# Performance work log

Measured on AMD Instinct MI355X. Metric: run time of the kernel, lower is better.

## Reference

```python
import jax, jax.numpy as jnp
import numpy as np

N_NODES = 50000


def _gcn_norm(edge_index, num_nodes):
    # PyG GCNConv default: add self-loops, symmetric deg^{-1/2} normalization.
    src, dst = edge_index[0], edge_index[1]
    loops = jnp.arange(num_nodes, dtype=src.dtype)
    src = jnp.concatenate([src, loops])
    dst = jnp.concatenate([dst, loops])
    ones = jnp.ones(src.shape[0], dtype=jnp.float32)
    deg = jax.ops.segment_sum(ones, dst, num_segments=num_nodes)
    dinv = jnp.where(deg > 0, jax.lax.rsqrt(deg), 0.0)
    norm = dinv[src] * dinv[dst]  # [E + N]
    return src, dst, norm


def _gcn_layer(x, src, dst, norm, W, b, num_nodes):
    h = x @ W                                   # [N, H]
    msg = h[src] * norm[:, None]                # gather + scale, [E+N, H]
    out = jax.ops.segment_sum(msg, dst, num_segments=num_nodes)  # scatter-add
    return out + b


def setup_inputs() -> dict:
    key = jax.random.key(0)
    ks = jax.random.split(key, 8)
    d_in, d_h = 128, 128
    x = jax.random.normal(ks[0], (N_NODES, d_in), dtype=jnp.float32)
    edge_index = jax.random.randint(ks[1], (2, 800000), 0, N_NODES, dtype=jnp.int64)
    s1 = 1.0 / np.sqrt(d_in)
    s2 = 1.0 / np.sqrt(d_h)
    W1 = jax.random.normal(ks[2], (d_in, d_h), dtype=jnp.float32) * s1
    b1 = jnp.zeros((d_h,), dtype=jnp.float32)
    W2 = jax.random.normal(ks[3], (d_h, d_h), dtype=jnp.float32) * s2
    b2 = jnp.zeros((d_h,), dtype=jnp.float32)
    Wl = jax.random.normal(ks[4], (d_h, 1), dtype=jnp.float32) * s2
    bl = jnp.zeros((1,), dtype=jnp.float32)
    return {"x": x, "edge_index": edge_index, "W1": W1, "b1": b1,
            "W2": W2, "b2": b2, "Wl": Wl, "bl": bl}


def reference(x, edge_index, W1, b1, W2, b2, Wl, bl):
    n = x.shape[0]
    src, dst, norm = _gcn_norm(edge_index, n)
    h = jax.nn.relu(_gcn_layer(x, src, dst, norm, W1, b1, n))
    # dropout is identity in eval mode
    h = _gcn_layer(h, src, dst, norm, W2, b2, n)
    return jax.nn.sigmoid(h @ Wl + bl)  # [N, 1]
```

## Files before the change

kernel.cpp:

```cpp
#include <hip/hip_runtime.h>
#include <math.h>

#define NN 50000
#define NE 800000
#define DD 128
#define NPAD 50048
#define NSLICE 6256
#define ELLW 64

typedef __attribute__((ext_vector_type(8))) short bf16x8;
typedef __attribute__((ext_vector_type(4))) float f32x4;

__device__ __forceinline__ int clampN(int v) {
  return v < 0 ? 0 : (v >= NN ? NN - 1 : v);
}

__device__ __forceinline__ unsigned short f2b(float f) {
  union { float f; unsigned int u; } x; x.f = f;
  unsigned int u = x.u;
  u += 0x7fffu + ((u >> 16) & 1u);
  return (unsigned short)(u >> 16);
}

__device__ __forceinline__ float blo(unsigned int v) {
  union { unsigned int u; float f; } a; a.u = v << 16; return a.f;
}
__device__ __forceinline__ float bhi(unsigned int v) {
  union { unsigned int u; float f; } a; a.u = v & 0xffff0000u; return a.f;
}


__global__ __launch_bounds__(256) void k_scatter_ell(
    const int* __restrict__ ei, int* __restrict__ cur, int* __restrict__ col) {
  int g = blockIdx.x & 7;
  int blk = blockIdx.x >> 3;
  int lo = g * NSLICE;
  int hi = min(lo + NSLICE, NN);
  for (int i = blk * 256 + threadIdx.x; i < NE; i += 256 * 256) {
    int d = clampN(ei[NE + i]);
    if (d >= lo && d < hi) {
      int s = clampN(ei[i]);
      int pos = atomicAdd(&cur[d], 1);
      if (pos < ELLW) col[d * ELLW + pos] = s;
    }
  }
}

__global__ void k_dinv(const int* __restrict__ cur, float* __restrict__ dinv, int n) {
  int i = blockIdx.x * blockDim.x + threadIdx.x;
  if (i < n) dinv[i] = rsqrtf(1.0f + (float)cur[i]);
}


__global__ __launch_bounds__(256) void k_prep_w(
    const float* __restrict__ W1, const float* __restrict__ W2,
    const float* __restrict__ b2, const float* __restrict__ Wl,
    const float* __restrict__ bl, unsigned short* __restrict__ Wt1,
    float* __restrict__ w2l, float* __restrict__ c0b) {
  __shared__ float part[2];
  if (blockIdx.x < 64) {
    int i = blockIdx.x * 256 + threadIdx.x;
    int n = i >> 7, k = i & 127;
    Wt1[i] = f2b(W1[k * DD + n]);
  } else if (threadIdx.x < DD) {
    int k = threadIdx.x;
    float acc = 0.f;
    for (int c = 0; c < DD; ++c) acc += W2[k * DD + c] * Wl[c];
    w2l[k] = acc;
    float pc = b2[k] * Wl[k];
#pragma unroll
    for (int off = 32; off > 0; off >>= 1) pc += __shfl_down(pc, off, 64);
    if ((k & 63) == 0) part[k >> 6] = pc;
    __syncthreads();
    if (k == 0) c0b[0] = part[0] + part[1] + bl[0];
  }
}


__global__ __launch_bounds__(256) void k_gemm_f32(
    const float* __restrict__ x, const unsigned short* __restrict__ Wt,
    const float* __restrict__ dinv, unsigned short* __restrict__ outb) {
  __shared__ char lds[16384 + 32768];
  char* Al = lds;
  char* Wl = lds + 16384;

  const int tid = threadIdx.x;
  const int row0 = blockIdx.x * 64;

  {
    const float4* src = (const float4*)x;
#pragma unroll
    for (int kk = 0; kk < 8; ++kk) {
      int idx = tid + kk * 256;
      int r = idx >> 5;
      int c4 = idx & 31;
      float4 v = make_float4(0.f, 0.f, 0.f, 0.f);
      if (row0 + r < NN) v = src[(size_t)(row0 + r) * 32 + c4];
      ushort4 u;
      u.x = f2b(v.x); u.y = f2b(v.y); u.z = f2b(v.z); u.w = f2b(v.w);
      int bo = r * 256 + c4 * 8;
      *(ushort4*)(Al + (bo ^ ((r & 7) << 4))) = u;
    }
  }
  {
    const uint4* src = (const uint4*)Wt;
    for (int idx = tid; idx < 2048; idx += 256) {
      int bo = idx * 16;
      int r = bo >> 8;
      *(uint4*)(Wl + (bo ^ ((r & 7) << 4))) = src[idx];
    }
  }
  __syncthreads();

  const int w = tid >> 6, lane = tid & 63;
  const int lr = lane & 15, lk = lane >> 4;

  bf16x8 af[4];
  {
    int ar = w * 16 + lr;
    int base = ar * 256 + lk * 16;
    int swz = (ar & 7) << 4;
#pragma unroll
    for (int k4 = 0; k4 < 4; ++k4)
      af[k4] = *(const bf16x8*)(Al + ((base + k4 * 64) ^ swz));
  }

  f32x4 accs[8];
#pragma unroll
  for (int n = 0; n < 8; ++n) {
    f32x4 acc = {0.f, 0.f, 0.f, 0.f};
    int br = n * 16 + lr;
    int bbase = br * 256 + lk * 16;
    int bswz = (br & 7) << 4;
#pragma unroll
    for (int k4 = 0; k4 < 4; ++k4) {
      bf16x8 bf = *(const bf16x8*)(Wl + ((bbase + k4 * 64) ^ bswz));
      acc = __builtin_amdgcn_mfma_f32_16x16x32_bf16(af[k4], bf, acc, 0, 0, 0);
    }
    accs[n] = acc;
  }

#pragma unroll
  for (int r = 0; r < 4; ++r) {
    int grow = row0 + w * 16 + lk * 4 + r;
    if (grow < NN) {
      float dv = dinv[grow];
#pragma unroll
      for (int n = 0; n < 8; ++n)
        outb[(size_t)grow * DD + n * 16 + lr] = f2b(accs[n][r] * dv);
    }
  }
}


__device__ __forceinline__ void acc8(float* acc, uint4 v) {
  acc[0] += blo(v.x);
  acc[1] += bhi(v.x);
  acc[2] += blo(v.y);
  acc[3] += bhi(v.y);
  acc[4] += blo(v.z);
  acc[5] += bhi(v.z);
  acc[6] += blo(v.w);
  acc[7] += bhi(v.w);
}

__global__ __launch_bounds__(256) void k_agg_relu_proj_ell(
    const uint4* __restrict__ tpb4, const float* __restrict__ dinv,
    const float* __restrict__ b, const float* __restrict__ w2l,
    const int* __restrict__ cur, const int* __restrict__ col,
    float* __restrict__ s_out) {
  int wid = threadIdx.x >> 6;
  int lane = threadIdx.x & 63;
  int d = blockIdx.x * 4 + wid;
  int il = lane & 7, g = lane >> 3;

  float acc[16];
#pragma unroll
  for (int j = 0; j < 16; ++j) acc[j] = 0.f;

  int deg = min(cur[d], ELLW);
  int base = d * ELLW;
  for (int e = g; e < deg; e += 8) {
    int s = col[base + e];
    uint4 v0 = tpb4[(size_t)s * 16 + il * 2];
    uint4 v1 = tpb4[(size_t)s * 16 + il * 2 + 1];
    acc8(acc, v0);
    acc8(acc + 8, v1);
  }
#pragma unroll
  for (int j = 0; j < 16; ++j) {
    acc[j] += __shfl_xor(acc[j], 8, 64);
    acc[j] += __shfl_xor(acc[j], 16, 64);
    acc[j] += __shfl_xor(acc[j], 32, 64);
  }
  uint4 s0 = tpb4[(size_t)d * 16 + il * 2];
  uint4 s1 = tpb4[(size_t)d * 16 + il * 2 + 1];
  acc8(acc, s0);
  acc8(acc + 8, s1);

  float dv = dinv[d];
  float p = 0.f;
#pragma unroll
  for (int q = 0; q < 4; ++q) {
    float4 bb = ((const float4*)b)[il * 4 + q];
    float4 ww = ((const float4*)w2l)[il * 4 + q];
    p = fmaf(fmaxf(fmaf(dv, acc[q * 4 + 0], bb.x), 0.f), ww.x, p);
    p = fmaf(fmaxf(fmaf(dv, acc[q * 4 + 1], bb.y), 0.f), ww.y, p);
    p = fmaf(fmaxf(fmaf(dv, acc[q * 4 + 2], bb.z), 0.f), ww.z, p);
    p = fmaf(fmaxf(fmaf(dv, acc[q * 4 + 3], bb.w), 0.f), ww.w, p);
  }
  p += __shfl_xor(p, 1, 64);
  p += __shfl_xor(p, 2, 64);
  p += __shfl_xor(p, 4, 64);
  if (lane == 0) s_out[d] = dv * p;
}


__global__ __launch_bounds__(256) void k_agg_scalar_ell(
    const float* __restrict__ s, const float* __restrict__ dinv,
    const float* __restrict__ c0b, const int* __restrict__ cur,
    const int* __restrict__ col, float* __restrict__ out) {
  int wid = threadIdx.x >> 6;
  int lane = threadIdx.x & 63;
  int q = lane & 15;
  int d = blockIdx.x * 16 + wid * 4 + (lane >> 4);

  int deg = min(cur[d], ELLW);
  int base = d * ELLW;
  float tot = 0.f;
  for (int e = q; e < deg; e += 16) tot += s[col[base + e]];
  tot += __shfl_xor(tot, 1, 64);
  tot += __shfl_xor(tot, 2, 64);
  tot += __shfl_xor(tot, 4, 64);
  tot += __shfl_xor(tot, 8, 64);
  if (q == 0) {
    float z = dinv[d] * (tot + s[d]) + c0b[0];
    out[d] = 1.f / (1.f + expf(-z));
  }
}


extern "C" void kernel_launch(void* const* d_in, const int* in_sizes, int n_in,
                              void* d_out, int out_size, void* d_ws, size_t ws_size,
                              hipStream_t stream) {
  const float* x = (const float*)d_in[0];
  const int* ei = (const int*)d_in[1];
  const float* W1 = (const float*)d_in[2];
  const float* b1 = (const float*)d_in[3];
  const float* W2 = (const float*)d_in[4];
  const float* b2 = (const float*)d_in[5];
  const float* Wl = (const float*)d_in[6];
  const float* bl = (const float*)d_in[7];
  float* out = (float*)d_out;

  char* ws = (char*)d_ws;
  size_t off = 0;
  auto alloc = [&](size_t bytes) -> char* {
    char* p = ws + off;
    off = (off + bytes + 255) & ~(size_t)255;
    return p;
  };
  int* cur = (int*)alloc(NN * sizeof(int));
  float* dinv = (float*)alloc(NN * sizeof(float));
  int* colell = (int*)alloc((size_t)NN * ELLW * sizeof(int));
  unsigned short* Wt1 = (unsigned short*)alloc(DD * DD * 2);
  float* w2l = (float*)alloc(DD * sizeof(float));
  float* c0b = (float*)alloc(sizeof(float));
  unsigned short* tpb = (unsigned short*)alloc((size_t)NPAD * DD * 2);
  float* sbuf = (float*)alloc(NN * sizeof(float));
  (void)ws_size;

  const int NB_N = (NN + 255) / 256;

  hipMemsetAsync(cur, 0, NN * sizeof(int), stream);
  k_scatter_ell<<<2048, 256, 0, stream>>>(ei, cur, colell);
  k_dinv<<<NB_N, 256, 0, stream>>>(cur, dinv, NN);

  k_prep_w<<<65, 256, 0, stream>>>(W1, W2, b2, Wl, bl, Wt1, w2l, c0b);

  k_gemm_f32<<<NPAD / 64, 256, 0, stream>>>(x, Wt1, dinv, tpb);
  k_agg_relu_proj_ell<<<NN / 4, 256, 0, stream>>>((const uint4*)tpb, dinv, b1, w2l,
                                                  cur, colell, sbuf);
  k_agg_scalar_ell<<<(NN + 15) / 16, 256, 0, stream>>>(sbuf, dinv, c0b, cur,
                                                       colell, out);
}
```

Measured before the change: 119.5 us.

## Fuse ELL scatter with GEMM launch and compute degree norms on the fly

The ELL adjacency scatter and the bf16 GEMM now run in one horizontally fused launch, with extra blocks doing the scatter. The GEMM no longer depends on degrees, so the two can overlap and the separate dinv kernel and buffer are removed. Per-edge normalization moves into the aggregation kernels: each edge recomputes rsqrt(1+deg[src]) from a gathered cur entry and applies it as an FMA. This trades launches and a serial dependency for an extra random 4-byte load and an rsqrt per edge.

```diff
diff --git a/kernel.cpp b/kernel.cpp
--- a/kernel.cpp
+++ b/kernel.cpp
@@ -7,6 +7,7 @@
 #define NPAD 50048
 #define NSLICE 6256
 #define ELLW 64
+#define NBG 782
 
 typedef __attribute__((ext_vector_type(8))) short bf16x8;
 typedef __attribute__((ext_vector_type(4))) float f32x4;
@@ -27,28 +28,6 @@
 }
 __device__ __forceinline__ float bhi(unsigned int v) {
   union { unsigned int u; float f; } a; a.u = v & 0xffff0000u; return a.f;
-}
-
-
-__global__ __launch_bounds__(256) void k_scatter_ell(
-    const int* __restrict__ ei, int* __restrict__ cur, int* __restrict__ col) {
-  int g = blockIdx.x & 7;
-  int blk = blockIdx.x >> 3;
-  int lo = g * NSLICE;
-  int hi = min(lo + NSLICE, NN);
-  for (int i = blk * 256 + threadIdx.x; i < NE; i += 256 * 256) {
-    int d = clampN(ei[NE + i]);
-    if (d >= lo && d < hi) {
-      int s = clampN(ei[i]);
-      int pos = atomicAdd(&cur[d], 1);
-      if (pos < ELLW) col[d * ELLW + pos] = s;
-    }
-  }
-}
-
-__global__ void k_dinv(const int* __restrict__ cur, float* __restrict__ dinv, int n) {
-  int i = blockIdx.x * blockDim.x + threadIdx.x;
-  if (i < n) dinv[i] = rsqrtf(1.0f + (float)cur[i]);
 }
 
 
@@ -77,10 +56,29 @@
 }
 
 
-__global__ __launch_bounds__(256) void k_gemm_f32(
+__global__ __launch_bounds__(256) void k_fused(
     const float* __restrict__ x, const unsigned short* __restrict__ Wt,
-    const float* __restrict__ dinv, unsigned short* __restrict__ outb) {
+    unsigned short* __restrict__ outb,
+    const int* __restrict__ ei, int* __restrict__ cur, int* __restrict__ col) {
   __shared__ char lds[16384 + 32768];
+
+  if (blockIdx.x >= NBG) {
+    int g = blockIdx.x & 7;
+    int j = blockIdx.x - NBG;
+    int blk = j >> 3;
+    int lo = g * NSLICE;
+    int hi = min(lo + NSLICE, NN);
+    for (int i = blk * 256 + threadIdx.x; i < NE; i += 256 * 256) {
+      int d = clampN(ei[NE + i]);
+      if (d >= lo && d < hi) {
+        int s = clampN(ei[i]);
+        int pos = atomicAdd(&cur[d], 1);
+        if (pos < ELLW) col[d * ELLW + pos] = s;
+      }
+    }
+    return;
+  }
+
   char* Al = lds;
   char* Wl = lds + 16384;
 
@@ -144,31 +142,29 @@
   for (int r = 0; r < 4; ++r) {
     int grow = row0 + w * 16 + lk * 4 + r;
     if (grow < NN) {
-      float dv = dinv[grow];
 #pragma unroll
       for (int n = 0; n < 8; ++n)
-        outb[(size_t)grow * DD + n * 16 + lr] = f2b(accs[n][r] * dv);
-    }
-  }
-}
-
-
-__device__ __forceinline__ void acc8(float* acc, uint4 v) {
-  acc[0] += blo(v.x);
-  acc[1] += bhi(v.x);
-  acc[2] += blo(v.y);
-  acc[3] += bhi(v.y);
-  acc[4] += blo(v.z);
-  acc[5] += bhi(v.z);
-  acc[6] += blo(v.w);
-  acc[7] += bhi(v.w);
+        outb[(size_t)grow * DD + n * 16 + lr] = f2b(accs[n][r]);
+    }
+  }
+}
+
+
+__device__ __forceinline__ void acc8m(float* acc, uint4 v, float m) {
+  acc[0] = fmaf(m, blo(v.x), acc[0]);
+  acc[1] = fmaf(m, bhi(v.x), acc[1]);
+  acc[2] = fmaf(m, blo(v.y), acc[2]);
+  acc[3] = fmaf(m, bhi(v.y), acc[3]);
+  acc[4] = fmaf(m, blo(v.z), acc[4]);
+  acc[5] = fmaf(m, bhi(v.z), acc[5]);
+  acc[6] = fmaf(m, blo(v.w), acc[6]);
+  acc[7] = fmaf(m, bhi(v.w), acc[7]);
 }
 
 __global__ __launch_bounds__(256) void k_agg_relu_proj_ell(
-    const uint4* __restrict__ tpb4, const float* __restrict__ dinv,
-    const float* __restrict__ b, const float* __restrict__ w2l,
-    const int* __restrict__ cur, const int* __restrict__ col,
-    float* __restrict__ s_out) {
+    const uint4* __restrict__ tpb4, const float* __restrict__ b,
+    const float* __restrict__ w2l, const int* __restrict__ cur,
+    const int* __restrict__ col, float* __restrict__ s_out) {
   int wid = threadIdx.x >> 6;
   int lane = threadIdx.x & 63;
   int d = blockIdx.x * 4 + wid;
@@ -178,14 +174,16 @@
 #pragma unroll
   for (int j = 0; j < 16; ++j) acc[j] = 0.f;
 
-  int deg = min(cur[d], ELLW);
+  int degd = cur[d];
+  int deg = min(degd, ELLW);
   int base = d * ELLW;
   for (int e = g; e < deg; e += 8) {
     int s = col[base + e];
+    float ds = rsqrtf(1.0f + (float)cur[s]);
     uint4 v0 = tpb4[(size_t)s * 16 + il * 2];
     uint4 v1 = tpb4[(size_t)s * 16 + il * 2 + 1];
-    acc8(acc, v0);
-    acc8(acc + 8, v1);
+    acc8m(acc, v0, ds);
+    acc8m(acc + 8, v1, ds);
   }
 #pragma unroll
   for (int j = 0; j < 16; ++j) {
@@ -193,12 +191,12 @@
     acc[j] += __shfl_xor(acc[j], 16, 64);
     acc[j] += __shfl_xor(acc[j], 32, 64);
   }
+  float dv = rsqrtf(1.0f + (float)degd);
   uint4 s0 = tpb4[(size_t)d * 16 + il * 2];
   uint4 s1 = tpb4[(size_t)d * 16 + il * 2 + 1];
-  acc8(acc, s0);
-  acc8(acc + 8, s1);
-
-  float dv = dinv[d];
+  acc8m(acc, s0, dv);
+  acc8m(acc + 8, s1, dv);
+
   float p = 0.f;
 #pragma unroll
   for (int q = 0; q < 4; ++q) {
@@ -217,15 +215,16 @@
 
 
 __global__ __launch_bounds__(256) void k_agg_scalar_ell(
-    const float* __restrict__ s, const float* __restrict__ dinv,
-    const float* __restrict__ c0b, const int* __restrict__ cur,
-    const int* __restrict__ col, float* __restrict__ out) {
+    const float* __restrict__ s, const float* __restrict__ c0b,
+    const int* __restrict__ cur, const int* __restrict__ col,
+    float* __restrict__ out) {
   int wid = threadIdx.x >> 6;
   int lane = threadIdx.x & 63;
   int q = lane & 15;
   int d = blockIdx.x * 16 + wid * 4 + (lane >> 4);
 
-  int deg = min(cur[d], ELLW);
+  int degd = cur[d];
+  int deg = min(degd, ELLW);
   int base = d * ELLW;
   float tot = 0.f;
   for (int e = q; e < deg; e += 16) tot += s[col[base + e]];
@@ -234,7 +233,8 @@
   tot += __shfl_xor(tot, 4, 64);
   tot += __shfl_xor(tot, 8, 64);
   if (q == 0) {
-    float z = dinv[d] * (tot + s[d]) + c0b[0];
+    float dv = rsqrtf(1.0f + (float)degd);
+    float z = dv * (tot + s[d]) + c0b[0];
     out[d] = 1.f / (1.f + expf(-z));
   }
 }
@@ -261,7 +261,6 @@
     return p;
   };
   int* cur = (int*)alloc(NN * sizeof(int));
-  float* dinv = (float*)alloc(NN * sizeof(float));
   int* colell = (int*)alloc((size_t)NN * ELLW * sizeof(int));
   unsigned short* Wt1 = (unsigned short*)alloc(DD * DD * 2);
   float* w2l = (float*)alloc(DD * sizeof(float));
@@ -270,17 +269,12 @@
   float* sbuf = (float*)alloc(NN * sizeof(float));
   (void)ws_size;
 
-  const int NB_N = (NN + 255) / 256;
-
   hipMemsetAsync(cur, 0, NN * sizeof(int), stream);
-  k_scatter_ell<<<2048, 256, 0, stream>>>(ei, cur, colell);
-  k_dinv<<<NB_N, 256, 0, stream>>>(cur, dinv, NN);
-
   k_prep_w<<<65, 256, 0, stream>>>(W1, W2, b2, Wl, bl, Wt1, w2l, c0b);
 
-  k_gemm_f32<<<NPAD / 64, 256, 0, stream>>>(x, Wt1, dinv, tpb);
-  k_agg_relu_proj_ell<<<NN / 4, 256, 0, stream>>>((const uint4*)tpb, dinv, b1, w2l,
+  k_fused<<<NBG + 2048, 256, 0, stream>>>(x, Wt1, tpb, ei, cur, colell);
+
+  k_agg_relu_proj_ell<<<NN / 4, 256, 0, stream>>>((const uint4*)tpb, b1, w2l,
                                                   cur, colell, sbuf);
-  k_agg_scalar_ell<<<(NN + 15) / 16, 256, 0, stream>>>(sbuf, dinv, c0b, cur,
-                                                       colell, out);
-}
+  k_agg_scalar_ell<<<(NN + 15) / 16, 256, 0, stream>>>(sbuf, c0b, cur, colell, out);
+}
```

After: 113.3 us. 1.05x faster.

## Store ELL columns as 16-bit indices and vectorize edge-list scatter loads

Applied to the files above, without the earlier changes.

Changes the ELL column array from 32-bit to 16-bit node indices, halving its footprint and the bytes written by the scatter and read by both aggregation kernels. The scatter kernel now reads destinations four at a time as int4 and loads sources only when one of the four falls in the block's slice. The aggregation accumulators become float2 vectors, which may allow packed adds, and the weight-prep kernel is launched earlier in the stream. A 16-bit index only works because node ids stay below 65536, so the change is tied to this problem size.

```diff
diff --git a/kernel.cpp b/kernel.cpp
--- a/kernel.cpp
+++ b/kernel.cpp
@@ -10,6 +10,7 @@
 
 typedef __attribute__((ext_vector_type(8))) short bf16x8;
 typedef __attribute__((ext_vector_type(4))) float f32x4;
+typedef __attribute__((ext_vector_type(2))) float f32x2;
 
 __device__ __forceinline__ int clampN(int v) {
   return v < 0 ? 0 : (v >= NN ? NN - 1 : v);
@@ -27,28 +28,6 @@
 }
 __device__ __forceinline__ float bhi(unsigned int v) {
   union { unsigned int u; float f; } a; a.u = v & 0xffff0000u; return a.f;
-}
-
-
-__global__ __launch_bounds__(256) void k_scatter_ell(
-    const int* __restrict__ ei, int* __restrict__ cur, int* __restrict__ col) {
-  int g = blockIdx.x & 7;
-  int blk = blockIdx.x >> 3;
-  int lo = g * NSLICE;
-  int hi = min(lo + NSLICE, NN);
-  for (int i = blk * 256 + threadIdx.x; i < NE; i += 256 * 256) {
-    int d = clampN(ei[NE + i]);
-    if (d >= lo && d < hi) {
-      int s = clampN(ei[i]);
-      int pos = atomicAdd(&cur[d], 1);
-      if (pos < ELLW) col[d * ELLW + pos] = s;
-    }
-  }
-}
-
-__global__ void k_dinv(const int* __restrict__ cur, float* __restrict__ dinv, int n) {
-  int i = blockIdx.x * blockDim.x + threadIdx.x;
-  if (i < n) dinv[i] = rsqrtf(1.0f + (float)cur[i]);
 }
 
 
@@ -77,6 +56,45 @@
 }
 
 
+__device__ __forceinline__ void scat1(int d, int s, int lo, int hi,
+                                      int* __restrict__ cur,
+                                      unsigned short* __restrict__ col) {
+  if (d >= lo && d < hi) {
+    int pos = atomicAdd(&cur[d], 1);
+    if (pos < ELLW) col[d * ELLW + pos] = (unsigned short)clampN(s);
+  }
+}
+
+__global__ __launch_bounds__(256) void k_scatter4(
+    const int4* __restrict__ src4, const int4* __restrict__ dst4,
+    int* __restrict__ cur, unsigned short* __restrict__ col) {
+  int g = blockIdx.x & 7;
+  int blk = blockIdx.x >> 3;
+  int lo = g * NSLICE;
+  int hi = min(lo + NSLICE, NN);
+  const int n4 = NE / 4;
+  for (int i = blk * 256 + threadIdx.x; i < n4; i += 256 * 256) {
+    int4 d4 = dst4[i];
+    d4.x = clampN(d4.x); d4.y = clampN(d4.y);
+    d4.z = clampN(d4.z); d4.w = clampN(d4.w);
+    bool any = (d4.x >= lo && d4.x < hi) | (d4.y >= lo && d4.y < hi) |
+               (d4.z >= lo && d4.z < hi) | (d4.w >= lo && d4.w < hi);
+    if (any) {
+      int4 s4 = src4[i];
+      scat1(d4.x, s4.x, lo, hi, cur, col);
+      scat1(d4.y, s4.y, lo, hi, cur, col);
+      scat1(d4.z, s4.z, lo, hi, cur, col);
+      scat1(d4.w, s4.w, lo, hi, cur, col);
+    }
+  }
+}
+
+__global__ void k_dinv(const int* __restrict__ cur, float* __restrict__ dinv, int n) {
+  int i = blockIdx.x * blockDim.x + threadIdx.x;
+  if (i < n) dinv[i] = rsqrtf(1.0f + (float)cur[i]);
+}
+
+
 __global__ __launch_bounds__(256) void k_gemm_f32(
     const float* __restrict__ x, const unsigned short* __restrict__ Wt,
     const float* __restrict__ dinv, unsigned short* __restrict__ outb) {
@@ -153,50 +171,52 @@
 }
 
 
-__device__ __forceinline__ void acc8(float* acc, uint4 v) {
-  acc[0] += blo(v.x);
-  acc[1] += bhi(v.x);
-  acc[2] += blo(v.y);
-  acc[3] += bhi(v.y);
-  acc[4] += blo(v.z);
-  acc[5] += bhi(v.z);
-  acc[6] += blo(v.w);
-  acc[7] += bhi(v.w);
+__device__ __forceinline__ void accp(f32x2* acc, uint4 v) {
+  f32x2 a0 = {blo(v.x), bhi(v.x)};
+  f32x2 a1 = {blo(v.y), bhi(v.y)};
+  f32x2 a2 = {blo(v.z), bhi(v.z)};
+  f32x2 a3 = {blo(v.w), bhi(v.w)};
+  acc[0] += a0;
+  acc[1] += a1;
+  acc[2] += a2;
+  acc[3] += a3;
 }
 
 __global__ __launch_bounds__(256) void k_agg_relu_proj_ell(
     const uint4* __restrict__ tpb4, const float* __restrict__ dinv,
     const float* __restrict__ b, const float* __restrict__ w2l,
-    const int* __restrict__ cur, const int* __restrict__ col,
+    const int* __restrict__ cur, const unsigned short* __restrict__ col,
     float* __restrict__ s_out) {
   int wid = threadIdx.x >> 6;
   int lane = threadIdx.x & 63;
   int d = blockIdx.x * 4 + wid;
   int il = lane & 7, g = lane >> 3;
 
-  float acc[16];
-#pragma unroll
-  for (int j = 0; j < 16; ++j) acc[j] = 0.f;
+  f32x2 acc[8];
+#pragma unroll
+  for (int j = 0; j < 8; ++j) acc[j] = (f32x2){0.f, 0.f};
 
   int deg = min(cur[d], ELLW);
-  int base = d * ELLW;
+  const unsigned short* crow = col + d * ELLW;
   for (int e = g; e < deg; e += 8) {
-    int s = col[base + e];
+    int s = crow[e];
     uint4 v0 = tpb4[(size_t)s * 16 + il * 2];
     uint4 v1 = tpb4[(size_t)s * 16 + il * 2 + 1];
-    acc8(acc, v0);
-    acc8(acc + 8, v1);
-  }
-#pragma unroll
-  for (int j = 0; j < 16; ++j) {
-    acc[j] += __shfl_xor(acc[j], 8, 64);
-    acc[j] += __shfl_xor(acc[j], 16, 64);
-    acc[j] += __shfl_xor(acc[j], 32, 64);
+    accp(acc, v0);
+    accp(acc + 4, v1);
+  }
+#pragma unroll
+  for (int j = 0; j < 8; ++j) {
+    float ax = acc[j].x, ay = acc[j].y;
+    ax += __shfl_xor(ax, 8, 64);  ay += __shfl_xor(ay, 8, 64);
+    ax += __shfl_xor(ax, 16, 64); ay += __shfl_xor(ay, 16, 64);
+    ax += __shfl_xor(ax, 32, 64); ay += __shfl_xor(ay, 32, 64);
+    acc[j].x = ax; acc[j].y = ay;
   }
   uint4 s0 = tpb4[(size_t)d * 16 + il * 2];
   uint4 s1 = tpb4[(size_t)d * 16 + il * 2 + 1];
-  acc8(acc, s0);
-  acc8(acc + 8, s1);
+  accp(acc, s0);
+  accp(acc + 4, s1);
 
   float dv = dinv[d];
   float p = 0.f;
@@ -204,10 +224,10 @@
   for (int q = 0; q < 4; ++q) {
     float4 bb = ((const float4*)b)[il * 4 + q];
     float4 ww = ((const float4*)w2l)[il * 4 + q];
-    p = fmaf(fmaxf(fmaf(dv, acc[q * 4 + 0], bb.x), 0.f), ww.x, p);
-    p = fmaf(fmaxf(fmaf(dv, acc[q * 4 + 1], bb.y), 0.f), ww.y, p);
-    p = fmaf(fmaxf(fmaf(dv, acc[q * 4 + 2], bb.z), 0.f), ww.z, p);
-    p = fmaf(fmaxf(fmaf(dv, acc[q * 4 + 3], bb.w), 0.f), ww.w, p);
+    p = fmaf(fmaxf(fmaf(dv, acc[2 * q].x, bb.x), 0.f), ww.x, p);
+    p = fmaf(fmaxf(fmaf(dv, acc[2 * q].y, bb.y), 0.f), ww.y, p);
+    p = fmaf(fmaxf(fmaf(dv, acc[2 * q + 1].x, bb.z), 0.f), ww.z, p);
+    p = fmaf(fmaxf(fmaf(dv, acc[2 * q + 1].y, bb.w), 0.f), ww.w, p);
   }
   p += __shfl_xor(p, 1, 64);
   p += __shfl_xor(p, 2, 64);
@@ -219,16 +239,16 @@
 __global__ __launch_bounds__(256) void k_agg_scalar_ell(
     const float* __restrict__ s, const float* __restrict__ dinv,
     const float* __restrict__ c0b, const int* __restrict__ cur,
-    const int* __restrict__ col, float* __restrict__ out) {
+    const unsigned short* __restrict__ col, float* __restrict__ out) {
   int wid = threadIdx.x >> 6;
   int lane = threadIdx.x & 63;
   int q = lane & 15;
   int d = blockIdx.x * 16 + wid * 4 + (lane >> 4);
 
   int deg = min(cur[d], ELLW);
-  int base = d * ELLW;
+  const unsigned short* crow = col + d * ELLW;
   float tot = 0.f;
-  for (int e = q; e < deg; e += 16) tot += s[col[base + e]];
+  for (int e = q; e < deg; e += 16) tot += s[crow[e]];
   tot += __shfl_xor(tot, 1, 64);
   tot += __shfl_xor(tot, 2, 64);
   tot += __shfl_xor(tot, 4, 64);
@@ -262,7 +282,7 @@
   };
   int* cur = (int*)alloc(NN * sizeof(int));
   float* dinv = (float*)alloc(NN * sizeof(float));
-  int* colell = (int*)alloc((size_t)NN * ELLW * sizeof(int));
+  unsigned short* colell = (unsigned short*)alloc((size_t)NN * ELLW * 2);
   unsigned short* Wt1 = (unsigned short*)alloc(DD * DD * 2);
   float* w2l = (float*)alloc(DD * sizeof(float));
   float* c0b = (float*)alloc(sizeof(float));
@@ -273,12 +293,14 @@
   const int NB_N = (NN + 255) / 256;
 
   hipMemsetAsync(cur, 0, NN * sizeof(int), stream);
-  k_scatter_ell<<<2048, 256, 0, stream>>>(ei, cur, colell);
+  k_prep_w<<<65, 256, 0, stream>>>(W1, W2, b2, Wl, bl, Wt1, w2l, c0b);
+
+  k_scatter4<<<2048, 256, 0, stream>>>((const int4*)ei, (const int4*)(ei + NE),
+                                       cur, colell);
   k_dinv<<<NB_N, 256, 0, stream>>>(cur, dinv, NN);
 
-  k_prep_w<<<65, 256, 0, stream>>>(W1, W2, b2, Wl, bl, Wt1, w2l, c0b);
-
   k_gemm_f32<<<NPAD / 64, 256, 0, stream>>>(x, Wt1, dinv, tpb);
+
   k_agg_relu_proj_ell<<<NN / 4, 256, 0, stream>>>((const uint4*)tpb, dinv, b1, w2l,
                                                   cur, colell, sbuf);
   k_agg_scalar_ell<<<(NN + 15) / 16, 256, 0, stream>>>(sbuf, dinv, c0b, cur,
```

After: 120.5 us. No clear change (+0.8%).
